# Optimization experiments

Measured on AMD Instinct MI355X. Metric: run time of the kernel, lower is better.

## Reference

```python
import jax, jax.numpy as jnp
import numpy as np

N, E = 10000, 160000
MUL0, MUL1, MUL2 = 64, 32, 16
DIM = MUL0 + MUL1 * 3 + MUL2 * 5          # 240
LAT, CPL, NTYPE = 128, 128, 95
NGATE = MUL1 + MUL2                        # 48 gate scalars
NCH = MUL0 + MUL1 + MUL2                   # 112 irrep channels
AVG_NEI = 16.0

# scaling_indices: per-channel index repeated over each irrep's dim
SCALE_IDX = np.concatenate([
    np.arange(MUL0),
    np.repeat(np.arange(MUL0, MUL0 + MUL1), 3),
    np.repeat(np.arange(MUL0 + MUL1, NCH), 5),
])


def _split(x, n):
    s = x[:, :MUL0]
    v1 = x[:, MUL0:MUL0 + MUL1 * 3].reshape(n, MUL1, 3)
    v2 = x[:, MUL0 + MUL1 * 3:].reshape(n, MUL2, 5)
    return s, v1, v2


def setup_inputs() -> dict:
    key = jax.random.key(0)
    ks = iter(jax.random.split(key, 48))
    rn = lambda *s: jax.random.normal(next(ks), s, dtype=jnp.float32)
    return dict(
        node_features=rn(N, DIM), edge_features=rn(E, DIM),
        latents=rn(E, LAT), msg_cpl=rn(N, CPL),
        node_onehot=jax.random.uniform(next(ks), (N, NTYPE), dtype=jnp.float32),
        wigner_D1=rn(E, 3, 3), wigner_D2=rn(E, 5, 5),
        so2_W0=rn(2 * MUL0, MUL0 + NGATE) * 0.08, so2_W1=rn(2 * MUL1, MUL1) * 0.12,
        so2_W2=rn(2 * MUL2, MUL2) * 0.17, so2_Ws=rn(LAT, NCH + NGATE) * 0.08,
        env_W=rn(LAT, NCH) * 0.08,
        post_W0=rn(MUL0, MUL0) * 0.12, post_b0=rn(MUL0) * 0.01,
        post_W1=rn(MUL1, MUL1) * 0.17, post_W2=rn(MUL2, MUL2) * 0.25,
        res_W0=rn(MUL0, MUL0) * 0.12, res_b0=rn(MUL0) * 0.01,
        res_W1=rn(MUL1, MUL1) * 0.17, res_W2=rn(MUL2, MUL2) * 0.25,
        cpl_W1=rn(CPL, CPL) * 0.08, cpl_b1=rn(CPL) * 0.01,
        cpl_W2=rn(CPL, NCH) * 0.08, cpl_b2=rn(NCH) * 0.01,
        gs_W=rn(MUL0, CPL) * 0.12, gs_b=rn(CPL) * 0.01,
        msg_W1=rn(2 * CPL, CPL) * 0.06, msg_b1=rn(CPL) * 0.01,
        msg_W2=rn(CPL, CPL) * 0.08, msg_b2=rn(CPL) * 0.01,
        ln_g=jnp.ones(CPL, jnp.float32), ln_b=jnp.zeros(CPL, jnp.float32),
        oh_w0=rn(MUL0, NTYPE) * 0.1, oh_w1=rn(MUL1, NTYPE) * 0.1, oh_w2=rn(MUL2, NTYPE) * 0.1,
        edge_index=jax.random.randint(next(ks), (2, E), 0, N),
    )


def _forward(node_features, edge_features, latents, msg_cpl, node_onehot,
             wigner_D1, wigner_D2, so2_W0, so2_W1, so2_W2, so2_Ws, env_W,
             post_W0, post_b0, post_W1, post_W2, res_W0, res_b0, res_W1, res_W2,
             cpl_W1, cpl_b1, cpl_W2, cpl_b2, gs_W, gs_b,
             msg_W1, msg_b1, msg_W2, msg_b2, ln_g, ln_b,
             oh_w0, oh_w1, oh_w2, edge_index):
    src = edge_index[0]
    ns, nv1, nv2 = _split(node_features, N)
    es, ev1, ev2 = _split(edge_features, E)
    # gather node feats to edges, concat with edge feats (per-l blocks)
    s_in = jnp.concatenate([ns[src], es], axis=1)                 # [E,128]
    v1_in = jnp.concatenate([nv1[src], ev1], axis=1)              # [E,64,3]
    v2_in = jnp.concatenate([nv2[src], ev2], axis=1)              # [E,32,5]
    # rotate into per-edge frame (Wigner D)
    v1_r = jnp.einsum('eij,ecj->eci', wigner_D1, v1_in)
    v2_r = jnp.einsum('eij,ecj->eci', wigner_D2, v2_in)
    # SO2 linear: shared channel mixing + latent-conditioned per-channel scales
    sc = latents @ so2_Ws                                         # [E,160]
    s_m = (s_in @ so2_W0) * sc[:, :MUL0 + NGATE]
    v1_m = jnp.einsum('eci,co->eoi', v1_r, so2_W1) * sc[:, MUL0 + NGATE:MUL0 + NGATE + MUL1, None]
    v2_m = jnp.einsum('eci,co->eoi', v2_r, so2_W2) * sc[:, MUL0 + NGATE + MUL1:, None]
    # rotate back
    v1_m = jnp.einsum('eji,eci->ecj', wigner_D1, v1_m)
    v2_m = jnp.einsum('eji,eci->ecj', wigner_D2, v2_m)
    # Gate activation
    s_act = jax.nn.silu(s_m[:, :MUL0])
    gates = jax.nn.sigmoid(s_m[:, MUL0:])
    v1_g = v1_m * gates[:, :MUL1, None]
    v2_g = v2_m * gates[:, MUL1:, None]
    # lin_post (per-l linear, bias on scalars)
    s_p = s_act @ post_W0 + post_b0
    v1_p = jnp.einsum('eci,co->eoi', v1_g, post_W1)
    v2_p = jnp.einsum('eci,co->eoi', v2_g, post_W2)
    # env element-wise weighting from latents
    w = latents @ env_W                                           # [E,112]
    s_p = s_p * w[:, :MUL0]
    v1_p = v1_p * w[:, MUL0:MUL0 + MUL1, None]
    v2_p = v2_p * w[:, MUL0 + MUL1:, None]
    msg = jnp.concatenate([s_p, v1_p.reshape(E, -1), v2_p.reshape(E, -1)], axis=1)
    # scatter-reduce to nodes + neighbor normalization
    agg = jax.ops.segment_sum(msg, src, num_segments=N) * (AVG_NEI ** -0.5)
    # coupling coefficients (per-channel, expanded by scaling_indices)
    coeffs = jax.nn.silu(msg_cpl @ cpl_W1 + cpl_b1) @ cpl_W2 + cpl_b2
    new_nf = agg * coeffs[:, SCALE_IDX]
    # coupling-channel update
    scal = new_nf[:, :MUL0] @ gs_W + gs_b
    h = jnp.concatenate([scal, msg_cpl], axis=1)
    upd = jax.nn.silu(h @ msg_W1 + msg_b1) @ msg_W2 + msg_b2
    mc = msg_cpl + upd
    mu = mc.mean(-1, keepdims=True)
    var = mc.var(-1, keepdims=True)
    msg_cpl_out = (mc - mu) * jax.lax.rsqrt(var + 1e-5) * ln_g + ln_b
    # residual mix with fixed logit-0 coefficients
    c = jax.nn.sigmoid(jnp.float32(0.0))
    c_old = jax.lax.rsqrt(c * c + 1.0)
    c_new = c * c_old
    rs = ns @ res_W0 + res_b0
    rv1 = jnp.einsum('eci,co->eoi', nv1, res_W1)
    rv2 = jnp.einsum('eci,co->eoi', nv2, res_W2)
    res = jnp.concatenate([rs, rv1.reshape(N, -1), rv2.reshape(N, -1)], axis=1)
    nf = c_new * new_nf + c_old * res
    # layer one-hot tensor product ('uvu' with 95x0e)
    inv = 1.0 / np.sqrt(NTYPE).astype(np.float32)
    g0 = (node_onehot @ oh_w0.T) * inv
    g1 = (node_onehot @ oh_w1.T) * inv
    g2 = (node_onehot @ oh_w2.T) * inv
    os_, ov1, ov2 = _split(nf, N)
    oh = jnp.concatenate([os_ * g0, (ov1 * g1[:, :, None]).reshape(N, -1),
                          (ov2 * g2[:, :, None]).reshape(N, -1)], axis=1)
    return nf + oh, msg_cpl_out


def reference(node_features, edge_features, latents, msg_cpl, node_onehot,
              wigner_D1, wigner_D2, so2_W0, so2_W1, so2_W2, so2_Ws, env_W,
              post_W0, post_b0, post_W1, post_W2, res_W0, res_b0, res_W1, res_W2,
              cpl_W1, cpl_b1, cpl_W2, cpl_b2, gs_W, gs_b,
              msg_W1, msg_b1, msg_W2, msg_b2, ln_g, ln_b,
              oh_w0, oh_w1, oh_w2, edge_index):
    return _forward(node_features, edge_features, latents, msg_cpl, node_onehot,
                    wigner_D1, wigner_D2, so2_W0, so2_W1, so2_W2, so2_Ws, env_W,
                    post_W0, post_b0, post_W1, post_W2, res_W0, res_b0, res_W1, res_W2,
                    cpl_W1, cpl_b1, cpl_W2, cpl_b2, gs_W, gs_b,
                    msg_W1, msg_b1, msg_W2, msg_b2, ln_g, ln_b,
                    oh_w0, oh_w1, oh_w2, edge_index)
```

## Files before the change

kernel.cpp:

```cpp
#include <hip/hip_runtime.h>

#define NN   10000
#define NE   160000
#define DIM  240
#define EB   16
#define NPB  16

typedef __bf16 bf16x8 __attribute__((ext_vector_type(8)));
typedef __bf16 bf16x4 __attribute__((ext_vector_type(4)));
typedef float  f32x4  __attribute__((ext_vector_type(4)));

__device__ __forceinline__ float sigf(float x) { return 1.0f / (1.0f + __expf(-x)); }

#define OFF_WB1 0
#define OFF_WB2 34816
#define OFF_W1  49152
#define OFF_W2  51200
#define OFF_PW0 51712
#define OFF_PW1 55808
#define OFF_PW2 56832
#define OHT_BYTE_OFF 131072
#define CNT_BYTE_OFF 196608
#define ROW_BYTE_OFF 237568
#define CUR_BYTE_OFF 282624
#define EID_BYTE_OFF 327680
#define MSG_BYTE_OFF 1048576

__global__ __launch_bounds__(256) void prep_kernel(
    const float* __restrict__ Ws, const float* __restrict__ We, const float* __restrict__ W0,
    const float* __restrict__ W1, const float* __restrict__ W2,
    const float* __restrict__ pW0, const float* __restrict__ pW1, const float* __restrict__ pW2,
    const float* __restrict__ w0g, const float* __restrict__ w1g, const float* __restrict__ w2g,
    __bf16* __restrict__ wsb, float* __restrict__ ohT)
{
    int tid = blockIdx.x * 256 + threadIdx.x;
    int stride = gridDim.x * 256;
    for (int idx = tid; idx < 17*4*512; idx += stride) {
        int j = idx & 7, lane = (idx >> 3) & 63, ks = (idx >> 9) & 3, nt = idx >> 11;
        int k = ks*32 + (lane >> 4)*8 + j, n = nt*16 + (lane & 15);
        float v = (n < 160) ? Ws[k*160 + n] : We[k*112 + (n - 160)];
        wsb[OFF_WB1 + idx] = (__bf16)v;
    }
    for (int idx = tid; idx < 7*4*512; idx += stride) {
        int j = idx & 7, lane = (idx >> 3) & 63, ks = (idx >> 9) & 3, nt = idx >> 11;
        int k = ks*32 + (lane >> 4)*8 + j, n = nt*16 + (lane & 15);
        wsb[OFF_WB2 + idx] = (__bf16)W0[k*112 + n];
    }
    for (int idx = tid; idx < 2*2*512; idx += stride) {
        int j = idx & 7, lane = (idx >> 3) & 63, ks = (idx >> 9) & 1, nt = idx >> 10;
        int k = ks*32 + (lane >> 4)*8 + j, n = nt*16 + (lane & 15);
        wsb[OFF_W1 + idx] = (__bf16)W1[k*32 + n];
    }
    for (int idx = tid; idx < 512; idx += stride) {
        int j = idx & 7, lane = (idx >> 3) & 63;
        int k = (lane >> 4)*8 + j, n = lane & 15;
        wsb[OFF_W2 + idx] = (__bf16)W2[k*16 + n];
    }
    for (int idx = tid; idx < 4*2*512; idx += stride) {
        int j = idx & 7, lane = (idx >> 3) & 63, ks = (idx >> 9) & 1, nt = idx >> 10;
        int k = ks*32 + (lane >> 4)*8 + j, n = nt*16 + (lane & 15);
        wsb[OFF_PW0 + idx] = (__bf16)pW0[k*64 + n];
    }
    for (int idx = tid; idx < 2*512; idx += stride) {
        int j = idx & 7, lane = (idx >> 3) & 63, nt = idx >> 9;
        int k = (lane >> 4)*8 + j, n = nt*16 + (lane & 15);
        wsb[OFF_PW1 + idx] = (__bf16)pW1[k*32 + n];
    }
    for (int idx = tid; idx < 512; idx += stride) {
        int j = idx & 7, lane = (idx >> 3) & 63;
        int k = (lane >> 4)*8 + j, n = lane & 15;
        wsb[OFF_PW2 + idx] = (k < 16) ? (__bf16)pW2[k*16 + n] : (__bf16)0.0f;
    }
    for (int idx = tid; idx < 96*112; idx += stride) {
        int k = idx / 112, n2 = idx - k*112;
        float v = 0.f;
        if (k < 95) {
            if (n2 < 64)      v = w0g[n2*95 + k];
            else if (n2 < 96) v = w1g[(n2-64)*95 + k];
            else              v = w2g[(n2-96)*95 + k];
        }
        ohT[idx] = v * 0.10259783521f;
    }
}

__global__ __launch_bounds__(256) void count_kernel(const int* __restrict__ src, int* __restrict__ cnt) {
    int e = blockIdx.x * 256 + threadIdx.x;
    if (e < NE) atomicAdd(&cnt[src[e]], 1);
}

__global__ __launch_bounds__(256) void scan_kernel(const int* __restrict__ cnt,
                                                   int* __restrict__ rowptr, int* __restrict__ cur) {
    __shared__ int part[256];
    int t = threadIdx.x;
    int base = t * 40;
    int local[40];
    int s = 0;
    #pragma unroll
    for (int i = 0; i < 40; i++) {
        int idx = base + i;
        int v = (idx < NN) ? cnt[idx] : 0;
        local[i] = s; s += v;
    }
    part[t] = s;
    __syncthreads();
    for (int off = 1; off < 256; off <<= 1) {
        int v = (t >= off) ? part[t - off] : 0;
        __syncthreads();
        part[t] += v;
        __syncthreads();
    }
    int pre = (t > 0) ? part[t - 1] : 0;
    #pragma unroll
    for (int i = 0; i < 40; i++) {
        int idx = base + i;
        if (idx < NN) { int r = pre + local[i]; rowptr[idx] = r; cur[idx] = r; }
    }
    if (t == 255) rowptr[NN] = part[255];
}

__global__ __launch_bounds__(256) void fill_kernel(const int* __restrict__ src,
                                                   int* __restrict__ cur, int* __restrict__ eidl) {
    int e = blockIdx.x * 256 + threadIdx.x;
    if (e < NE) {
        int slot = atomicAdd(&cur[src[e]], 1);
        eidl[slot] = e;
    }
}

__global__ __launch_bounds__(256) void agg_kernel(
    const __bf16* __restrict__ msg, const int* __restrict__ rowptr,
    const int* __restrict__ eidl, float* __restrict__ out0)
{
    int wid = threadIdx.x >> 6, lane = threadIdx.x & 63;
    int node = blockIdx.x * 4 + wid;
    if (node >= NN || lane >= 60) return;
    int beg = rowptr[node], end = rowptr[node + 1];
    float a0 = 0.f, a1 = 0.f, a2 = 0.f, a3 = 0.f;
    int i = beg;
    for (; i + 4 <= end; i += 4) {
        int e0 = eidl[i], e1 = eidl[i+1], e2 = eidl[i+2], e3 = eidl[i+3];
        bf16x4 v0 = *(const bf16x4*)(msg + (size_t)e0*240 + lane*4);
        bf16x4 v1 = *(const bf16x4*)(msg + (size_t)e1*240 + lane*4);
        bf16x4 v2 = *(const bf16x4*)(msg + (size_t)e2*240 + lane*4);
        bf16x4 v3 = *(const bf16x4*)(msg + (size_t)e3*240 + lane*4);
        a0 += (float)v0[0] + (float)v1[0] + (float)v2[0] + (float)v3[0];
        a1 += (float)v0[1] + (float)v1[1] + (float)v2[1] + (float)v3[1];
        a2 += (float)v0[2] + (float)v1[2] + (float)v2[2] + (float)v3[2];
        a3 += (float)v0[3] + (float)v1[3] + (float)v2[3] + (float)v3[3];
    }
    for (; i < end; i++) {
        int e = eidl[i];
        bf16x4 v = *(const bf16x4*)(msg + (size_t)e*240 + lane*4);
        a0 += (float)v[0]; a1 += (float)v[1]; a2 += (float)v[2]; a3 += (float)v[3];
    }
    float4 r = { a0, a1, a2, a3 };
    *(float4*)(out0 + (size_t)node*240 + lane*4) = r;
}

__global__ __launch_bounds__(256, 4) void edge_mfma_kernel(
    const float* __restrict__ nf, const float* __restrict__ ef,
    const float* __restrict__ latg, const float* __restrict__ D1g, const float* __restrict__ D2g,
    const float* __restrict__ pb0, const int* __restrict__ srcg,
    const __bf16* __restrict__ wsb, float* agg, __bf16* __restrict__ msgout)
{
    __shared__ __align__(16) unsigned char pool[39936];
    __bf16* Cb   = (__bf16*)(pool + 0);
    __bf16* aLat = (__bf16*)(pool + 12544);
    __bf16* aSin = (__bf16*)(pool + 16640);
    __bf16* v1m  = (__bf16*)(pool + 12544);
    __bf16* v2m  = (__bf16*)(pool + 16384);
    __bf16* vt1  = (__bf16*)(pool + 20736);
    __bf16* vt2  = (__bf16*)(pool + 27136);
    __bf16* aV1g = (__bf16*)(pool + 20736);
    __bf16* aV2g = (__bf16*)(pool + 23808);
    float*  d1s  = (float*)(pool + 32512);
    float*  d2s  = (float*)(pool + 33088);
    float*  gts  = (float*)(pool + 32512);
    __bf16* aSact= (__bf16*)(pool + 35648);
    float*  e1s  = (float*)(pool + 37696);
    float*  e2s  = (float*)(pool + 38272);

    const int t    = threadIdx.x;
    const int wid  = t >> 6, lane = t & 63;
    const int e0   = blockIdx.x * EB;

    for (int idx = t; idx < 144; idx += 256) d1s[idx] = D1g[e0*9  + idx];
    for (int idx = t; idx < 400; idx += 256) d2s[idx] = D2g[e0*25 + idx];
    {
        int e = t >> 4, half = (t >> 3) & 1, cq = t & 7;
        const float* base = half ? (ef + (size_t)(e0 + e)*240 + 64 + cq*12)
                                 : (nf + (size_t)srcg[e0 + e]*240 + 64 + cq*12);
        float4 f0 = *(const float4*)base;
        float4 f1 = *(const float4*)(base + 4);
        float4 f2 = *(const float4*)(base + 8);
        float f[12] = {f0.x,f0.y,f0.z,f0.w,f1.x,f1.y,f1.z,f1.w,f2.x,f2.y,f2.z,f2.w};
        int c = half*32 + cq*4;
        __bf16* dst = vt1 + e*200 + c;
        #pragma unroll
        for (int i = 0; i < 3; i++) {
            bf16x4 v = {(__bf16)f[i], (__bf16)f[3+i], (__bf16)f[6+i], (__bf16)f[9+i]};
            *(bf16x4*)(dst + i*64) = v;
        }
    }
    if (t < 128) {
        int e = t >> 3, half = (t >> 2) & 1, cq = t & 3;
        const float* base = half ? (ef + (size_t)(e0 + e)*240 + 160 + cq*20)
                                 : (nf + (size_t)srcg[e0 + e]*240 + 160 + cq*20);
        float f[20];
        #pragma unroll
        for (int k = 0; k < 5; k++) {
            float4 q4 = *(const float4*)(base + k*4);
            f[4*k] = q4.x; f[4*k+1] = q4.y; f[4*k+2] = q4.z; f[4*k+3] = q4.w;
        }
        int c = half*16 + cq*4;
        __bf16* dst = vt2 + e*168 + c;
        #pragma unroll
        for (int z = 0; z < 5; z++) {
            bf16x4 v = {(__bf16)f[z], (__bf16)f[5+z], (__bf16)f[10+z], (__bf16)f[15+z]};
            *(bf16x4*)(dst + z*32) = v;
        }
    }
    {
        int ks = t >> 6, l2 = t & 63, e = l2 & 15;
        int k0 = ks*32 + (l2 >> 4)*8;
        {
            const float4* p4 = (const float4*)(latg + (size_t)(e0 + e)*128 + k0);
            float4 f0 = p4[0], f1 = p4[1];
            bf16x8 v;
            v[0]=(__bf16)f0.x; v[1]=(__bf16)f0.y; v[2]=(__bf16)f0.z; v[3]=(__bf16)f0.w;
            v[4]=(__bf16)f1.x; v[5]=(__bf16)f1.y; v[6]=(__bf16)f1.z; v[7]=(__bf16)f1.w;
            *(bf16x8*)(aLat + t*8) = v;
        }
        {
            const float* s2 = (k0 < 64) ? (nf + (size_t)srcg[e0 + e]*240 + k0)
                                        : (ef + (size_t)(e0 + e)*240 + (k0 - 64));
            const float4* p4 = (const float4*)s2;
            float4 f0 = p4[0], f1 = p4[1];
            bf16x8 v;
            v[0]=(__bf16)f0.x; v[1]=(__bf16)f0.y; v[2]=(__bf16)f0.z; v[3]=(__bf16)f0.w;
            v[4]=(__bf16)f1.x; v[5]=(__bf16)f1.y; v[6]=(__bf16)f1.z; v[7]=(__bf16)f1.w;
            *(bf16x8*)(aSin + t*8) = v;
        }
    }
    __syncthreads();

    {
        int col16 = lane & 15, ebase = (lane >> 4)*4;
        bf16x8 aL[4], aS[4];
        #pragma unroll
        for (int ks = 0; ks < 4; ks++) {
            aL[ks] = *(const bf16x8*)(aLat + (ks*64 + lane)*8);
            aS[ks] = *(const bf16x8*)(aSin + (ks*64 + lane)*8);
        }
        #pragma unroll
        for (int it = 0; it < 6; it++) {
            int nt = wid + it*4;
            bool isLat = nt < 17;
            const __bf16* bB = isLat ? (wsb + OFF_WB1 + nt*2048)
                                     : (wsb + OFF_WB2 + (nt - 17)*2048);
            f32x4 acc = {0.f, 0.f, 0.f, 0.f};
            #pragma unroll
            for (int ks = 0; ks < 4; ks++) {
                bf16x8 b = *(const bf16x8*)(bB + (ks*64 + lane)*8);
                acc = __builtin_amdgcn_mfma_f32_16x16x32_bf16(isLat ? aL[ks] : aS[ks], b, acc, 0, 0, 0);
            }
            int col = (isLat ? nt*16 : 272 + (nt - 17)*16) + col16;
            #pragma unroll
            for (int r = 0; r < 4; r++) Cb[(ebase + r)*392 + col] = (__bf16)acc[r];
        }
    }
    for (int idx = t; idx < 544; idx += 256) {
        if (idx < 144) {
            int e = idx / 9, r = idx - e*9, i = r / 3, k = r - i*3;
            const float* d = d1s + e*9;
            e1s[idx] = d[i*3+0]*d[0*3+k] + d[i*3+1]*d[1*3+k] + d[i*3+2]*d[2*3+k];
        } else {
            int j = idx - 144;
            int e = j / 25, r = j - e*25, i = r / 5, k = r - i*5;
            const float* d = d2s + e*25;
            float a = 0.f;
            #pragma unroll
            for (int tt = 0; tt < 5; tt++) a += d[i*5+tt] * d[tt*5+k];
            e2s[j] = a;
        }
    }
    __syncthreads();

    {
        int col16 = lane & 15, er = lane & 15, q8 = (lane >> 4)*8, ebase = (lane >> 4)*4;
        for (int p = wid; p < 11; p += 4) {
            f32x4 acc = {0.f, 0.f, 0.f, 0.f};
            if (p < 6) {
                int i = p >> 1, nt = p & 1;
                #pragma unroll
                for (int ks = 0; ks < 2; ks++) {
                    bf16x8 a = *(const bf16x8*)(vt1 + er*200 + i*64 + ks*32 + q8);
                    bf16x8 b = *(const bf16x8*)(wsb + OFF_W1 + ((nt*2 + ks)*64 + lane)*8);
                    acc = __builtin_amdgcn_mfma_f32_16x16x32_bf16(a, b, acc, 0, 0, 0);
                }
                int col = nt*16 + col16;
                #pragma unroll
                for (int r = 0; r < 4; r++) v1m[(i*16 + ebase + r)*40 + col] = (__bf16)acc[r];
            } else {
                int i = p - 6;
                bf16x8 a = *(const bf16x8*)(vt2 + er*168 + i*32 + q8);
                bf16x8 b = *(const bf16x8*)(wsb + OFF_W2 + lane*8);
                acc = __builtin_amdgcn_mfma_f32_16x16x32_bf16(a, b, acc, 0, 0, 0);
                #pragma unroll
                for (int r = 0; r < 4; r++) v2m[(i*16 + ebase + r)*24 + col16] = (__bf16)acc[r];
            }
        }
    }
    if (t < 128) {
        int ks = t >> 6, l2 = t & 63, e = l2 & 15, o0 = ks*32 + (l2 >> 4)*8;
        bf16x8 v;
        #pragma unroll
        for (int j = 0; j < 8; j++) {
            int o = o0 + j;
            float x = (float)Cb[e*392 + 272 + o] * (float)Cb[e*392 + o];
            v[j] = (__bf16)(x * sigf(x));
        }
        *(bf16x8*)(aSact + t*8) = v;
    }
    for (int idx = t; idx < 768; idx += 256) {
        int e = idx / 48, o = idx - e*48;
        float x = (float)Cb[e*392 + 336 + o] * (float)Cb[e*392 + 64 + o];
        gts[e*49 + o] = sigf(x);
    }
    __syncthreads();

    for (int idx = t; idx < 512; idx += 256) {
        if (idx < 192) {
            int i = idx >> 6, l2 = idx & 63, e = l2 & 15, c0 = (l2 >> 4)*8;
            float z0 = e1s[e*9 + i*3], z1 = e1s[e*9 + i*3 + 1], z2 = e1s[e*9 + i*3 + 2];
            bf16x8 m0 = *(const bf16x8*)(v1m + (0*16 + e)*40 + c0);
            bf16x8 m1 = *(const bf16x8*)(v1m + (1*16 + e)*40 + c0);
            bf16x8 m2 = *(const bf16x8*)(v1m + (2*16 + e)*40 + c0);
            bf16x8 s8 = *(const bf16x8*)(Cb + e*392 + 112 + c0);
            bf16x8 v;
            #pragma unroll
            for (int j = 0; j < 8; j++) {
                float g = gts[e*49 + c0 + j];
                float a = z0*(float)m0[j] + z1*(float)m1[j] + z2*(float)m2[j];
                v[j] = (__bf16)(g * (float)s8[j] * a);
            }
            *(bf16x8*)(aV1g + idx*8) = v;
        } else {
            int idx2 = idx - 192;
            int i = idx2 >> 6, l2 = idx2 & 63, e = l2 & 15, c0 = (l2 >> 4)*8;
            bf16x8 v;
            if (c0 < 16) {
                const float* ee = e2s + e*25 + i*5;
                float z0 = ee[0], z1 = ee[1], z2 = ee[2], z3 = ee[3], z4 = ee[4];
                bf16x8 m0 = *(const bf16x8*)(v2m + (0*16 + e)*24 + c0);
                bf16x8 m1 = *(const bf16x8*)(v2m + (1*16 + e)*24 + c0);
                bf16x8 m2 = *(const bf16x8*)(v2m + (2*16 + e)*24 + c0);
                bf16x8 m3 = *(const bf16x8*)(v2m + (3*16 + e)*24 + c0);
                bf16x8 m4 = *(const bf16x8*)(v2m + (4*16 + e)*24 + c0);
                bf16x8 s8 = *(const bf16x8*)(Cb + e*392 + 144 + c0);
                #pragma unroll
                for (int j = 0; j < 8; j++) {
                    float g = gts[e*49 + 32 + c0 + j];
                    float a = z0*(float)m0[j] + z1*(float)m1[j] + z2*(float)m2[j]
                            + z3*(float)m3[j] + z4*(float)m4[j];
                    v[j] = (__bf16)(g * (float)s8[j] * a);
                }
            } else {
                #pragma unroll
                for (int j = 0; j < 8; j++) v[j] = (__bf16)0.0f;
            }
            *(bf16x8*)(aV2g + idx2*8) = v;
        }
    }
    __syncthreads();

    {
        int col16 = lane & 15, ebase = (lane >> 4)*4;
        for (int p = wid; p < 15; p += 4) {
            f32x4 acc = {0.f, 0.f, 0.f, 0.f};
            if (p < 4) {
                int nt = p;
                #pragma unroll
                for (int ks = 0; ks < 2; ks++) {
                    bf16x8 a = *(const bf16x8*)(aSact + (ks*64 + lane)*8);
                    bf16x8 b = *(const bf16x8*)(wsb + OFF_PW0 + ((nt*2 + ks)*64 + lane)*8);
                    acc = __builtin_amdgcn_mfma_f32_16x16x32_bf16(a, b, acc, 0, 0, 0);
                }
                int o = nt*16 + col16;
                float bias = pb0[o];
                #pragma unroll
                for (int r = 0; r < 4; r++) {
                    int e = ebase + r;
                    float val = (acc[r] + bias) * (float)Cb[e*392 + 160 + o];
                    if (msgout) msgout[(size_t)(e0 + e)*240 + o] = (__bf16)val;
                    else        atomicAdd(agg + (size_t)srcg[e0 + e]*240 + o, val);
                }
            } else if (p < 10) {
                int q = p - 4, i = q >> 1, nt = q & 1;
                bf16x8 a = *(const bf16x8*)(aV1g + (i*64 + lane)*8);
                bf16x8 b = *(const bf16x8*)(wsb + OFF_PW1 + (nt*64 + lane)*8);
                acc = __builtin_amdgcn_mfma_f32_16x16x32_bf16(a, b, acc, 0, 0, 0);
                int o = nt*16 + col16;
                #pragma unroll
                for (int r = 0; r < 4; r++) {
                    int e = ebase + r;
                    float val = acc[r] * (float)Cb[e*392 + 224 + o];
                    if (msgout) msgout[(size_t)(e0 + e)*240 + 64 + o*3 + i] = (__bf16)val;
                    else        atomicAdd(agg + (size_t)srcg[e0 + e]*240 + 64 + o*3 + i, val);
                }
            } else {
                int i = p - 10;
                bf16x8 a = *(const bf16x8*)(aV2g + (i*64 + lane)*8);
                bf16x8 b = *(const bf16x8*)(wsb + OFF_PW2 + lane*8);
                acc = __builtin_amdgcn_mfma_f32_16x16x32_bf16(a, b, acc, 0, 0, 0);
                #pragma unroll
                for (int r = 0; r < 4; r++) {
                    int e = ebase + r;
                    float val = acc[r] * (float)Cb[e*392 + 256 + col16];
                    if (msgout) msgout[(size_t)(e0 + e)*240 + 160 + col16*5 + i] = (__bf16)val;
                    else        atomicAdd(agg + (size_t)srcg[e0 + e]*240 + 160 + col16*5 + i, val);
                }
            }
        }
    }
}

__global__ __launch_bounds__(256, 2) void node_kernel(
    const float* __restrict__ nf, const float* __restrict__ mcplg,
    const float* __restrict__ ohg,
    const float* __restrict__ cW1, const float* __restrict__ cb1,
    const float* __restrict__ cW2, const float* __restrict__ cb2,
    const float* __restrict__ gsW, const float* __restrict__ gsb,
    const float* __restrict__ mW1, const float* __restrict__ mb1,
    const float* __restrict__ mW2, const float* __restrict__ mb2,
    const float* __restrict__ lng, const float* __restrict__ lnb,
    const float* __restrict__ rW0, const float* __restrict__ rb0,
    const float* __restrict__ rW1, const float* __restrict__ rW2,
    const float* __restrict__ ohT, float* out0, float* out1)
{
    __shared__ __align__(16) unsigned char pool[68608];
    float* mcp  = (float*)(pool + 0);
    float* ohv  = (float*)(pool + 8192);
    float* nsr  = (float*)(pool + 14336);
    float* anew = (float*)(pool + 29696);
    float* t12  = (float*)(pool + 45056);
    float* cfg  = (float*)(pool + 53248);
    float* scm  = (float*)(pool + 60416);

    const int t  = threadIdx.x;
    const int g  = t >> 7;
    const int o  = t & 127;
    const int nb = g * 8;
    const int n0 = blockIdx.x * NPB;

    for (int idx = t; idx < NPB * 128; idx += 256) {
        int n = idx >> 7, k = idx & 127;
        mcp[n*128 + k] = mcplg[(n0 + n) * 128 + k];
    }
    for (int idx = t; idx < NPB * 96; idx += 256) {
        int n = idx / 96, k = idx - n * 96;
        ohv[n*96 + k] = (k < 95) ? ohg[(n0 + n) * 95 + k] : 0.f;
    }
    for (int idx = t; idx < NPB * 240; idx += 256) {
        int n = idx / 240, k = idx - n * 240;
        nsr[n*240 + k]  = nf[(n0 + n) * DIM + k];
        anew[n*240 + k] = out0[(n0 + n) * DIM + k];
    }
    __syncthreads();

    {
        float a[8]; float b = cb1[o];
        #pragma unroll
        for (int i = 0; i < 8; i++) a[i] = b;
        #pragma unroll 2
        for (int k4 = 0; k4 < 32; k4++) {
            float w0 = cW1[(4*k4+0)*128 + o], w1 = cW1[(4*k4+1)*128 + o],
                  w2 = cW1[(4*k4+2)*128 + o], w3 = cW1[(4*k4+3)*128 + o];
            #pragma unroll
            for (int i = 0; i < 8; i++) {
                float4 m = *(const float4*)&mcp[(nb+i)*128 + 4*k4];
                a[i] += m.x*w0 + m.y*w1 + m.z*w2 + m.w*w3;
            }
        }
        #pragma unroll
        for (int i = 0; i < 8; i++) { float x = a[i]; t12[(nb+i)*128 + o] = x * sigf(x); }
    }
    __syncthreads();

    if (o < 112) {
        float a[8]; float b = cb2[o];
        #pragma unroll
        for (int i = 0; i < 8; i++) a[i] = b;
        #pragma unroll 2
        for (int k4 = 0; k4 < 32; k4++) {
            float w0 = cW2[(4*k4+0)*112 + o], w1 = cW2[(4*k4+1)*112 + o],
                  w2 = cW2[(4*k4+2)*112 + o], w3 = cW2[(4*k4+3)*112 + o];
            #pragma unroll
            for (int i = 0; i < 8; i++) {
                float4 m = *(const float4*)&t12[(nb+i)*128 + 4*k4];
                a[i] += m.x*w0 + m.y*w1 + m.z*w2 + m.w*w3;
            }
        }
        #pragma unroll
        for (int i = 0; i < 8; i++) cfg[(nb+i)*112 + o] = a[i];
    }
    __syncthreads();

    for (int idx = t; idx < NPB * 240; idx += 256) {
        int n = idx / 240, d = idx - n * 240;
        int ch = (d < 64) ? d : (d < 160 ? 64 + (d - 64) / 3 : 96 + (d - 160) / 5);
        anew[n*240 + d] *= 0.25f * cfg[n*112 + ch];
    }
    __syncthreads();

    {
        float a[8]; float b = gsb[o];
        #pragma unroll
        for (int i = 0; i < 8; i++) a[i] = b;
        #pragma unroll 2
        for (int k4 = 0; k4 < 16; k4++) {
            float w0 = gsW[(4*k4+0)*128 + o], w1 = gsW[(4*k4+1)*128 + o],
                  w2 = gsW[(4*k4+2)*128 + o], w3 = gsW[(4*k4+3)*128 + o];
            #pragma unroll
            for (int i = 0; i < 8; i++) {
                float4 m = *(const float4*)&anew[(nb+i)*240 + 4*k4];
                a[i] += m.x*w0 + m.y*w1 + m.z*w2 + m.w*w3;
            }
        }
        #pragma unroll
        for (int i = 0; i < 8; i++) scm[(nb+i)*128 + o] = a[i];
    }
    __syncthreads();

    {
        float a[8]; float b = mb1[o];
        #pragma unroll
        for (int i = 0; i < 8; i++) a[i] = b;
        #pragma unroll 2
        for (int k4 = 0; k4 < 32; k4++) {
            float w0 = mW1[(4*k4+0)*128 + o], w1 = mW1[(4*k4+1)*128 + o],
                  w2 = mW1[(4*k4+2)*128 + o], w3 = mW1[(4*k4+3)*128 + o];
            #pragma unroll
            for (int i = 0; i < 8; i++) {
                float4 m = *(const float4*)&scm[(nb+i)*128 + 4*k4];
                a[i] += m.x*w0 + m.y*w1 + m.z*w2 + m.w*w3;
            }
        }
        #pragma unroll 2
        for (int k4 = 0; k4 < 32; k4++) {
            float w0 = mW1[(128+4*k4+0)*128 + o], w1 = mW1[(128+4*k4+1)*128 + o],
                  w2 = mW1[(128+4*k4+2)*128 + o], w3 = mW1[(128+4*k4+3)*128 + o];
            #pragma unroll
            for (int i = 0; i < 8; i++) {
                float4 m = *(const float4*)&mcp[(nb+i)*128 + 4*k4];
                a[i] += m.x*w0 + m.y*w1 + m.z*w2 + m.w*w3;
            }
        }
        #pragma unroll
        for (int i = 0; i < 8; i++) { float x = a[i]; t12[(nb+i)*128 + o] = x * sigf(x); }
    }
    __syncthreads();

    {
        float a[8]; float b = mb2[o];
        #pragma unroll
        for (int i = 0; i < 8; i++) a[i] = b;
        #pragma unroll 2
        for (int k4 = 0; k4 < 32; k4++) {
            float w0 = mW2[(4*k4+0)*128 + o], w1 = mW2[(4*k4+1)*128 + o],
                  w2 = mW2[(4*k4+2)*128 + o], w3 = mW2[(4*k4+3)*128 + o];
            #pragma unroll
            for (int i = 0; i < 8; i++) {
                float4 m = *(const float4*)&t12[(nb+i)*128 + 4*k4];
                a[i] += m.x*w0 + m.y*w1 + m.z*w2 + m.w*w3;
            }
        }
        #pragma unroll
        for (int i = 0; i < 8; i++) scm[(nb+i)*128 + o] = mcp[(nb+i)*128 + o] + a[i];
    }
    __syncthreads();

    {
        int n = t >> 4, l = t & 15;
        float x[8]; float s = 0.f, ss = 0.f;
        #pragma unroll
        for (int i = 0; i < 8; i++) { x[i] = scm[n*128 + l + 16*i]; s += x[i]; ss += x[i]*x[i]; }
        #pragma unroll
        for (int off = 8; off > 0; off >>= 1) {
            s  += __shfl_down(s,  off, 16);
            ss += __shfl_down(ss, off, 16);
        }
        s  = __shfl(s, 0, 16);
        ss = __shfl(ss, 0, 16);
        float mu   = s * (1.f / 128.f);
        float var  = ss * (1.f / 128.f) - mu * mu;
        float rstd = rsqrtf(var + 1e-5f);
        float* op = out1 + (n0 + n) * 128;
        #pragma unroll
        for (int i = 0; i < 8; i++) {
            int c = l + 16*i;
            op[c] = (x[i] - mu) * rstd * lng[c] + lnb[c];
        }
    }

    if (o < 112) {
        float a[8] = {0.f,0.f,0.f,0.f,0.f,0.f,0.f,0.f};
        #pragma unroll 2
        for (int k4 = 0; k4 < 24; k4++) {
            float w0 = ohT[(4*k4+0)*112 + o], w1 = ohT[(4*k4+1)*112 + o],
                  w2 = ohT[(4*k4+2)*112 + o], w3 = ohT[(4*k4+3)*112 + o];
            #pragma unroll
            for (int i = 0; i < 8; i++) {
                float4 m = *(const float4*)&ohv[(nb+i)*96 + 4*k4];
                a[i] += m.x*w0 + m.y*w1 + m.z*w2 + m.w*w3;
            }
        }
        #pragma unroll
        for (int i = 0; i < 8; i++) cfg[(nb+i)*112 + o] = a[i];
    }
    __syncthreads();

    const float c_new = 0.4472135955f;
    const float c_old = 0.8944271910f;
    for (int idx = t; idx < NPB * 240; idx += 256) {
        int n = idx / 240, d = idx - n * 240;
        float res, gg;
        if (d < 64) {
            float acc = rb0[d];
            #pragma unroll 4
            for (int c = 0; c < 64; c++) acc += nsr[n*240 + c] * rW0[c * 64 + d];
            res = acc; gg = cfg[n*112 + d];
        } else if (d < 160) {
            int dd = d - 64, oo = dd / 3, j = dd - oo * 3;
            float acc = 0.f;
            #pragma unroll 4
            for (int c = 0; c < 32; c++) acc += nsr[n*240 + 64 + c*3 + j] * rW1[c * 32 + oo];
            res = acc; gg = cfg[n*112 + 64 + oo];
        } else {
            int dd = d - 160, oo = dd / 5, j = dd - oo * 5;
            float acc = 0.f;
            #pragma unroll 4
            for (int c = 0; c < 16; c++) acc += nsr[n*240 + 160 + c*5 + j] * rW2[c * 16 + oo];
            res = acc; gg = cfg[n*112 + 96 + oo];
        }
        float v = c_new * anew[n*240 + d] + c_old * res;
        out0[(n0 + n) * DIM + d] = v * (1.f + gg);
    }
}

extern "C" void kernel_launch(void* const* d_in, const int* in_sizes, int n_in,
                              void* d_out, int out_size, void* d_ws, size_t ws_size,
                              hipStream_t stream) {
    const float* nf      = (const float*)d_in[0];
    const float* ef      = (const float*)d_in[1];
    const float* lat     = (const float*)d_in[2];
    const float* mcpl    = (const float*)d_in[3];
    const float* ohot    = (const float*)d_in[4];
    const float* D1      = (const float*)d_in[5];
    const float* D2      = (const float*)d_in[6];
    const float* so2_W0  = (const float*)d_in[7];
    const float* so2_W1  = (const float*)d_in[8];
    const float* so2_W2  = (const float*)d_in[9];
    const float* so2_Ws  = (const float*)d_in[10];
    const float* env_W   = (const float*)d_in[11];
    const float* post_W0 = (const float*)d_in[12];
    const float* post_b0 = (const float*)d_in[13];
    const float* post_W1 = (const float*)d_in[14];
    const float* post_W2 = (const float*)d_in[15];
    const float* res_W0  = (const float*)d_in[16];
    const float* res_b0  = (const float*)d_in[17];
    const float* res_W1  = (const float*)d_in[18];
    const float* res_W2  = (const float*)d_in[19];
    const float* cpl_W1  = (const float*)d_in[20];
    const float* cpl_b1  = (const float*)d_in[21];
    const float* cpl_W2  = (const float*)d_in[22];
    const float* cpl_b2  = (const float*)d_in[23];
    const float* gs_W    = (const float*)d_in[24];
    const float* gs_b    = (const float*)d_in[25];
    const float* msg_W1  = (const float*)d_in[26];
    const float* msg_b1  = (const float*)d_in[27];
    const float* msg_W2  = (const float*)d_in[28];
    const float* msg_b2  = (const float*)d_in[29];
    const float* ln_g    = (const float*)d_in[30];
    const float* ln_b    = (const float*)d_in[31];
    const float* oh_w0   = (const float*)d_in[32];
    const float* oh_w1   = (const float*)d_in[33];
    const float* oh_w2   = (const float*)d_in[34];
    const int*   eidx    = (const int*)d_in[35];

    float* out0 = (float*)d_out;
    float* out1 = (float*)d_out + (size_t)NN * DIM;
    char*   wsB = (char*)d_ws;
    __bf16* wsb = (__bf16*)d_ws;
    float*  ohT = (float*)(wsB + OHT_BYTE_OFF);

    const size_t need = (size_t)MSG_BYTE_OFF + (size_t)NE * 240 * 2;
    const bool planA = ws_size >= need;

    (void)hipMemsetAsync(out0, 0, (size_t)NN * DIM * sizeof(float), stream);

    prep_kernel<<<56, 256, 0, stream>>>(so2_Ws, env_W, so2_W0, so2_W1, so2_W2,
                                        post_W0, post_W1, post_W2,
                                        oh_w0, oh_w1, oh_w2, wsb, ohT);

    if (planA) {
        int*    cnt  = (int*)(wsB + CNT_BYTE_OFF);
        int*    row  = (int*)(wsB + ROW_BYTE_OFF);
        int*    cur  = (int*)(wsB + CUR_BYTE_OFF);
        int*    eidl = (int*)(wsB + EID_BYTE_OFF);
        __bf16* msg  = (__bf16*)(wsB + MSG_BYTE_OFF);

        (void)hipMemsetAsync(cnt, 0, 10240 * sizeof(int), stream);
        count_kernel<<<(NE + 255) / 256, 256, 0, stream>>>(eidx, cnt);
        scan_kernel<<<1, 256, 0, stream>>>(cnt, row, cur);
        fill_kernel<<<(NE + 255) / 256, 256, 0, stream>>>(eidx, cur, eidl);

        edge_mfma_kernel<<<NE / EB, 256, 0, stream>>>(
            nf, ef, lat, D1, D2, post_b0, eidx, wsb, out0, msg);

        agg_kernel<<<(NN + 3) / 4, 256, 0, stream>>>(msg, row, eidl, out0);
    } else {
        edge_mfma_kernel<<<NE / EB, 256, 0, stream>>>(
            nf, ef, lat, D1, D2, post_b0, eidx, wsb, out0, nullptr);
    }

    node_kernel<<<NN / NPB, 256, 0, stream>>>(
        nf, mcpl, ohot, cpl_W1, cpl_b1, cpl_W2, cpl_b2, gs_W, gs_b,
        msg_W1, msg_b1, msg_W2, msg_b2, ln_g, ln_b,
        res_W0, res_b0, res_W1, res_W2, ohT, out0, out1);
}
```

Before: 699.6 us.

## Process edges in source-sorted order and reduce per-block before atomics, dropping message buffer

Edges are now processed in CSR order keyed by source node, so each block's 16 edges mostly share a few source nodes. The per-edge messages are written into a shared-memory tile and segment-reduced by source, then flushed with one atomicAdd per run. This removes the bf16 message round-trip through global memory and the separate aggregation kernel. The count kernel is folded into the prep kernel as extra blocks, and the first two B-weight tiles are prefetched into registers. In exchange, inputs are gathered indirectly through the edge list, so reads of ef, latents and the D matrices become less coalesced, and the kernel still relies on float atomics.

```diff
diff --git a/kernel.cpp b/kernel.cpp
--- a/kernel.cpp
+++ b/kernel.cpp
@@ -24,17 +24,24 @@
 #define ROW_BYTE_OFF 237568
 #define CUR_BYTE_OFF 282624
 #define EID_BYTE_OFF 327680
-#define MSG_BYTE_OFF 1048576
 
 __global__ __launch_bounds__(256) void prep_kernel(
     const float* __restrict__ Ws, const float* __restrict__ We, const float* __restrict__ W0,
     const float* __restrict__ W1, const float* __restrict__ W2,
     const float* __restrict__ pW0, const float* __restrict__ pW1, const float* __restrict__ pW2,
     const float* __restrict__ w0g, const float* __restrict__ w1g, const float* __restrict__ w2g,
-    __bf16* __restrict__ wsb, float* __restrict__ ohT)
+    __bf16* __restrict__ wsb, float* __restrict__ ohT,
+    const int* __restrict__ src, int* __restrict__ cnt)
 {
+    if (blockIdx.x >= 56) {
+        if (cnt) {
+            int e = (blockIdx.x - 56) * 256 + threadIdx.x;
+            if (e < NE) atomicAdd(&cnt[src[e]], 1);
+        }
+        return;
+    }
     int tid = blockIdx.x * 256 + threadIdx.x;
-    int stride = gridDim.x * 256;
+    const int stride = 56 * 256;
     for (int idx = tid; idx < 17*4*512; idx += stride) {
         int j = idx & 7, lane = (idx >> 3) & 63, ks = (idx >> 9) & 3, nt = idx >> 11;
         int k = ks*32 + (lane >> 4)*8 + j, n = nt*16 + (lane & 15);
@@ -81,11 +88,6 @@
         }
         ohT[idx] = v * 0.10259783521f;
     }
-}
-
-__global__ __launch_bounds__(256) void count_kernel(const int* __restrict__ src, int* __restrict__ cnt) {
-    int e = blockIdx.x * 256 + threadIdx.x;
-    if (e < NE) atomicAdd(&cnt[src[e]], 1);
 }
 
 __global__ __launch_bounds__(256) void scan_kernel(const int* __restrict__ cnt,
@@ -127,48 +129,19 @@
     }
 }
 
-__global__ __launch_bounds__(256) void agg_kernel(
-    const __bf16* __restrict__ msg, const int* __restrict__ rowptr,
-    const int* __restrict__ eidl, float* __restrict__ out0)
-{
-    int wid = threadIdx.x >> 6, lane = threadIdx.x & 63;
-    int node = blockIdx.x * 4 + wid;
-    if (node >= NN || lane >= 60) return;
-    int beg = rowptr[node], end = rowptr[node + 1];
-    float a0 = 0.f, a1 = 0.f, a2 = 0.f, a3 = 0.f;
-    int i = beg;
-    for (; i + 4 <= end; i += 4) {
-        int e0 = eidl[i], e1 = eidl[i+1], e2 = eidl[i+2], e3 = eidl[i+3];
-        bf16x4 v0 = *(const bf16x4*)(msg + (size_t)e0*240 + lane*4);
-        bf16x4 v1 = *(const bf16x4*)(msg + (size_t)e1*240 + lane*4);
-        bf16x4 v2 = *(const bf16x4*)(msg + (size_t)e2*240 + lane*4);
-        bf16x4 v3 = *(const bf16x4*)(msg + (size_t)e3*240 + lane*4);
-        a0 += (float)v0[0] + (float)v1[0] + (float)v2[0] + (float)v3[0];
-        a1 += (float)v0[1] + (float)v1[1] + (float)v2[1] + (float)v3[1];
-        a2 += (float)v0[2] + (float)v1[2] + (float)v2[2] + (float)v3[2];
-        a3 += (float)v0[3] + (float)v1[3] + (float)v2[3] + (float)v3[3];
-    }
-    for (; i < end; i++) {
-        int e = eidl[i];
-        bf16x4 v = *(const bf16x4*)(msg + (size_t)e*240 + lane*4);
-        a0 += (float)v[0]; a1 += (float)v[1]; a2 += (float)v[2]; a3 += (float)v[3];
-    }
-    float4 r = { a0, a1, a2, a3 };
-    *(float4*)(out0 + (size_t)node*240 + lane*4) = r;
-}
-
 __global__ __launch_bounds__(256, 4) void edge_mfma_kernel(
     const float* __restrict__ nf, const float* __restrict__ ef,
     const float* __restrict__ latg, const float* __restrict__ D1g, const float* __restrict__ D2g,
     const float* __restrict__ pb0, const int* __restrict__ srcg,
-    const __bf16* __restrict__ wsb, float* agg, __bf16* __restrict__ msgout)
+    const int* __restrict__ eidl, const __bf16* __restrict__ wsb, float* agg)
 {
-    __shared__ __align__(16) unsigned char pool[39936];
+    __shared__ __align__(16) unsigned char pool[40064];
     __bf16* Cb   = (__bf16*)(pool + 0);
     __bf16* aLat = (__bf16*)(pool + 12544);
     __bf16* aSin = (__bf16*)(pool + 16640);
     __bf16* v1m  = (__bf16*)(pool + 12544);
     __bf16* v2m  = (__bf16*)(pool + 16384);
+    __bf16* mtile= (__bf16*)(pool + 12544);
     __bf16* vt1  = (__bf16*)(pool + 20736);
     __bf16* vt2  = (__bf16*)(pool + 27136);
     __bf16* aV1g = (__bf16*)(pool + 20736);
@@ -179,17 +152,41 @@
     __bf16* aSact= (__bf16*)(pool + 35648);
     float*  e1s  = (float*)(pool + 37696);
     float*  e2s  = (float*)(pool + 38272);
+    int*    srcs = (int*)  (pool + 39872);
+    int*    eids = (int*)  (pool + 39936);
 
     const int t    = threadIdx.x;
     const int wid  = t >> 6, lane = t & 63;
     const int e0   = blockIdx.x * EB;
 
-    for (int idx = t; idx < 144; idx += 256) d1s[idx] = D1g[e0*9  + idx];
-    for (int idx = t; idx < 400; idx += 256) d2s[idx] = D2g[e0*25 + idx];
+    #define EIDX(e) (eidl ? eidl[e0 + (e)] : (e0 + (e)))
+
+    bf16x8 bpre[8];
+    {
+        const __bf16* b0 = wsb + OFF_WB1 + wid*2048;
+        const __bf16* b1 = wsb + OFF_WB1 + (wid + 4)*2048;
+        #pragma unroll
+        for (int ks = 0; ks < 4; ks++) {
+            bpre[ks]     = *(const bf16x8*)(b0 + (ks*64 + lane)*8);
+            bpre[4 + ks] = *(const bf16x8*)(b1 + (ks*64 + lane)*8);
+        }
+    }
+
+    if (t < 16) { int ee = EIDX(t); eids[t] = ee; srcs[t] = srcg[ee]; }
+
+    for (int idx = t; idx < 144; idx += 256) {
+        int e = idx / 9; int ee = EIDX(e);
+        d1s[idx] = D1g[(size_t)ee*9 + (idx - e*9)];
+    }
+    for (int idx = t; idx < 400; idx += 256) {
+        int e = idx / 25; int ee = EIDX(e);
+        d2s[idx] = D2g[(size_t)ee*25 + (idx - e*25)];
+    }
     {
         int e = t >> 4, half = (t >> 3) & 1, cq = t & 7;
-        const float* base = half ? (ef + (size_t)(e0 + e)*240 + 64 + cq*12)
-                                 : (nf + (size_t)srcg[e0 + e]*240 + 64 + cq*12);
+        int ee = EIDX(e);
+        const float* base = half ? (ef + (size_t)ee*240 + 64 + cq*12)
+                                 : (nf + (size_t)srcg[ee]*240 + 64 + cq*12);
         float4 f0 = *(const float4*)base;
         float4 f1 = *(const float4*)(base + 4);
         float4 f2 = *(const float4*)(base + 8);
@@ -204,8 +201,9 @@
     }
     if (t < 128) {
         int e = t >> 3, half = (t >> 2) & 1, cq = t & 3;
-        const float* base = half ? (ef + (size_t)(e0 + e)*240 + 160 + cq*20)
-                                 : (nf + (size_t)srcg[e0 + e]*240 + 160 + cq*20);
+        int ee = EIDX(e);
+        const float* base = half ? (ef + (size_t)ee*240 + 160 + cq*20)
+                                 : (nf + (size_t)srcg[ee]*240 + 160 + cq*20);
         float f[20];
         #pragma unroll
         for (int k = 0; k < 5; k++) {
@@ -223,8 +221,9 @@
     {
         int ks = t >> 6, l2 = t & 63, e = l2 & 15;
         int k0 = ks*32 + (l2 >> 4)*8;
+        int ee = EIDX(e);
         {
-            const float4* p4 = (const float4*)(latg + (size_t)(e0 + e)*128 + k0);
+            const float4* p4 = (const float4*)(latg + (size_t)ee*128 + k0);
             float4 f0 = p4[0], f1 = p4[1];
             bf16x8 v;
             v[0]=(__bf16)f0.x; v[1]=(__bf16)f0.y; v[2]=(__bf16)f0.z; v[3]=(__bf16)f0.w;
@@ -232,8 +231,8 @@
             *(bf16x8*)(aLat + t*8) = v;
         }
         {
-            const float* s2 = (k0 < 64) ? (nf + (size_t)srcg[e0 + e]*240 + k0)
-                                        : (ef + (size_t)(e0 + e)*240 + (k0 - 64));
+            const float* s2 = (k0 < 64) ? (nf + (size_t)srcg[ee]*240 + k0)
+                                        : (ef + (size_t)ee*240 + (k0 - 64));
             const float4* p4 = (const float4*)s2;
             float4 f0 = p4[0], f1 = p4[1];
             bf16x8 v;
@@ -261,7 +260,9 @@
             f32x4 acc = {0.f, 0.f, 0.f, 0.f};
             #pragma unroll
             for (int ks = 0; ks < 4; ks++) {
-                bf16x8 b = *(const bf16x8*)(bB + (ks*64 + lane)*8);
+                bf16x8 b;
+                if (it < 2) b = bpre[it*4 + ks];
+                else        b = *(const bf16x8*)(bB + (ks*64 + lane)*8);
                 acc = __builtin_amdgcn_mfma_f32_16x16x32_bf16(isLat ? aL[ks] : aS[ks], b, acc, 0, 0, 0);
             }
             int col = (isLat ? nt*16 : 272 + (nt - 17)*16) + col16;
@@ -392,8 +393,8 @@
                 for (int r = 0; r < 4; r++) {
                     int e = ebase + r;
                     float val = (acc[r] + bias) * (float)Cb[e*392 + 160 + o];
-                    if (msgout) msgout[(size_t)(e0 + e)*240 + o] = (__bf16)val;
-                    else        atomicAdd(agg + (size_t)srcg[e0 + e]*240 + o, val);
+                    if (eidl) mtile[e*248 + o] = (__bf16)val;
+                    else      atomicAdd(agg + (size_t)srcs[e]*240 + o, val);
                 }
             } else if (p < 10) {
                 int q = p - 4, i = q >> 1, nt = q & 1;
@@ -405,8 +406,8 @@
                 for (int r = 0; r < 4; r++) {
                     int e = ebase + r;
                     float val = acc[r] * (float)Cb[e*392 + 224 + o];
-                    if (msgout) msgout[(size_t)(e0 + e)*240 + 64 + o*3 + i] = (__bf16)val;
-                    else        atomicAdd(agg + (size_t)srcg[e0 + e]*240 + 64 + o*3 + i, val);
+                    if (eidl) mtile[e*248 + 64 + o*3 + i] = (__bf16)val;
+                    else      atomicAdd(agg + (size_t)srcs[e]*240 + 64 + o*3 + i, val);
                 }
             } else {
                 int i = p - 10;
@@ -417,12 +418,31 @@
                 for (int r = 0; r < 4; r++) {
                     int e = ebase + r;
                     float val = acc[r] * (float)Cb[e*392 + 256 + col16];
-                    if (msgout) msgout[(size_t)(e0 + e)*240 + 160 + col16*5 + i] = (__bf16)val;
-                    else        atomicAdd(agg + (size_t)srcg[e0 + e]*240 + 160 + col16*5 + i, val);
+                    if (eidl) mtile[e*248 + 160 + col16*5 + i] = (__bf16)val;
+                    else      atomicAdd(agg + (size_t)srcs[e]*240 + 160 + col16*5 + i, val);
                 }
             }
         }
     }
+
+    if (eidl) {
+        __syncthreads();
+        if (t < 240) {
+            float s = 0.f;
+            int prev = srcs[0];
+            #pragma unroll
+            for (int e = 0; e < EB; e++) {
+                int sn = srcs[e];
+                if (sn != prev) {
+                    atomicAdd(agg + (size_t)prev*240 + t, s);
+                    s = 0.f; prev = sn;
+                }
+                s += (float)mtile[e*248 + t];
+            }
+            atomicAdd(agg + (size_t)prev*240 + t, s);
+        }
+    }
+    #undef EIDX
 }
 
 __global__ __launch_bounds__(256, 2) void node_kernel(
@@ -694,34 +714,32 @@
     __bf16* wsb = (__bf16*)d_ws;
     float*  ohT = (float*)(wsB + OHT_BYTE_OFF);
 
-    const size_t need = (size_t)MSG_BYTE_OFF + (size_t)NE * 240 * 2;
-    const bool planA = ws_size >= need;
+    const size_t needA = (size_t)EID_BYTE_OFF + (size_t)NE * sizeof(int);
+    const bool planA = ws_size >= needA;
 
     (void)hipMemsetAsync(out0, 0, (size_t)NN * DIM * sizeof(float), stream);
 
-    prep_kernel<<<56, 256, 0, stream>>>(so2_Ws, env_W, so2_W0, so2_W1, so2_W2,
-                                        post_W0, post_W1, post_W2,
-                                        oh_w0, oh_w1, oh_w2, wsb, ohT);
-
     if (planA) {
-        int*    cnt  = (int*)(wsB + CNT_BYTE_OFF);
-        int*    row  = (int*)(wsB + ROW_BYTE_OFF);
-        int*    cur  = (int*)(wsB + CUR_BYTE_OFF);
-        int*    eidl = (int*)(wsB + EID_BYTE_OFF);
-        __bf16* msg  = (__bf16*)(wsB + MSG_BYTE_OFF);
+        int* cnt  = (int*)(wsB + CNT_BYTE_OFF);
+        int* row  = (int*)(wsB + ROW_BYTE_OFF);
+        int* cur  = (int*)(wsB + CUR_BYTE_OFF);
+        int* eidl = (int*)(wsB + EID_BYTE_OFF);
 
         (void)hipMemsetAsync(cnt, 0, 10240 * sizeof(int), stream);
-        count_kernel<<<(NE + 255) / 256, 256, 0, stream>>>(eidx, cnt);
+        prep_kernel<<<56 + (NE + 255) / 256, 256, 0, stream>>>(
+            so2_Ws, env_W, so2_W0, so2_W1, so2_W2, post_W0, post_W1, post_W2,
+            oh_w0, oh_w1, oh_w2, wsb, ohT, eidx, cnt);
         scan_kernel<<<1, 256, 0, stream>>>(cnt, row, cur);
         fill_kernel<<<(NE + 255) / 256, 256, 0, stream>>>(eidx, cur, eidl);
 
         edge_mfma_kernel<<<NE / EB, 256, 0, stream>>>(
-            nf, ef, lat, D1, D2, post_b0, eidx, wsb, out0, msg);
-
-        agg_kernel<<<(NN + 3) / 4, 256, 0, stream>>>(msg, row, eidl, out0);
+            nf, ef, lat, D1, D2, post_b0, eidx, eidl, wsb, out0);
     } else {
+        prep_kernel<<<56, 256, 0, stream>>>(
+            so2_Ws, env_W, so2_W0, so2_W1, so2_W2, post_W0, post_W1, post_W2,
+            oh_w0, oh_w1, oh_w2, wsb, ohT, eidx, nullptr);
         edge_mfma_kernel<<<NE / EB, 256, 0, stream>>>(
-            nf, ef, lat, D1, D2, post_b0, eidx, wsb, out0, nullptr);
+            nf, ef, lat, D1, D2, post_b0, eidx, nullptr, wsb, out0);
     }
 
     node_kernel<<<NN / NPB, 256, 0, stream>>>(
```

Result: no change. 695.3 us (-0.6%).
